# Performance work log

Measured on AMD Instinct MI355X. Metric: run time of the kernel, lower is better.

The kernel has to match this reference:

```python
import jax, jax.numpy as jnp
import numpy as np
import math

B, R, D = 1, 2, 256
NH, NL, NP, ZA = 8, 1, 8, 4
H = W = 128
Q = H * W
HD = D // NH


def _bilinear(v, loc, Hl, Wl):
    # v: [BH, Hl*Wl, hd]; loc: [BH, Q, P, 2] normalized to [0,1]
    x = loc[..., 0] * Wl - 0.5
    y = loc[..., 1] * Hl - 0.5
    x0f = jnp.floor(x); y0f = jnp.floor(y)
    wx = (x - x0f)[..., None]; wy = (y - y0f)[..., None]
    x0 = x0f.astype(jnp.int32); y0 = y0f.astype(jnp.int32)
    def corner(iy, ix):
        valid = (iy >= 0) & (iy < Hl) & (ix >= 0) & (ix < Wl)
        idx = jnp.clip(iy, 0, Hl - 1) * Wl + jnp.clip(ix, 0, Wl - 1)
        g = jax.vmap(lambda vb, ib: vb[ib])(v, idx)  # [BH,Q,P,hd]
        return g * valid[..., None].astype(v.dtype)
    g00 = corner(y0, x0); g01 = corner(y0, x0 + 1)
    g10 = corner(y0 + 1, x0); g11 = corner(y0 + 1, x0 + 1)
    return (g00 * (1 - wx) + g01 * wx) * (1 - wy) + (g10 * (1 - wx) + g11 * wx) * wy


def setup_inputs() -> dict:
    key = jax.random.key(0)
    ks = jax.random.split(key, 12)
    query = jax.random.normal(ks[0], (B, Q, D), jnp.float32)
    value = jax.random.normal(ks[1], (B * R, Q, D), jnp.float32)
    reference_points = jax.random.uniform(ks[2], (R, Q, ZA, 2), jnp.float32)
    spatial_shapes = jnp.array([[H, W]], jnp.int32)
    # sampling_offsets: zero-ish weight + directional grid bias (as in init_weights)
    W_off = 0.01 * jax.random.normal(ks[3], (NH * NL * NP * 2, D), jnp.float32)
    thetas = jnp.arange(NH, dtype=jnp.float32) * (2.0 * math.pi / NH)
    grid = jnp.stack([jnp.cos(thetas), jnp.sin(thetas)], -1)
    grid = grid / jnp.max(jnp.abs(grid), axis=-1, keepdims=True)
    grid = jnp.tile(grid[:, None, None, :], (1, NL, NP, 1))
    grid = grid * (jnp.arange(1, NP + 1, dtype=jnp.float32)[None, None, :, None])
    b_off = grid.reshape(-1)
    W_attn = 0.01 * jax.random.normal(ks[4], (NH * NL * NP, D), jnp.float32)
    b_attn = 0.01 * jax.random.normal(ks[5], (NH * NL * NP,), jnp.float32)
    s = 1.0 / np.sqrt(D)
    W_val = s * jax.random.normal(ks[6], (D, D), jnp.float32)
    b_val = jnp.zeros((D,), jnp.float32)
    W_out = s * jax.random.normal(ks[7], (D, D), jnp.float32)
    b_out = jnp.zeros((D,), jnp.float32)
    return {"query": query, "value": value, "reference_points": reference_points,
            "spatial_shapes": spatial_shapes, "W_off": W_off, "b_off": b_off,
            "W_attn": W_attn, "b_attn": b_attn, "W_val": W_val, "b_val": b_val,
            "W_out": W_out, "b_out": b_out}


def reference(query, value, reference_points, spatial_shapes,
              W_off, b_off, W_attn, b_attn, W_val, b_val, W_out, b_out):
    shapes = np.asarray(spatial_shapes)  # static level shapes
    residual = query
    Bq, nq, d = query.shape
    Rr, _, za, _ = reference_points.shape
    # rebatch query/reference_points over histories -> batch Bq*Rr (== value batch)
    q = jnp.broadcast_to(query[:, None], (Bq, Rr, nq, d)).reshape(Bq * Rr, nq, d)
    rp = jnp.broadcast_to(reference_points[None], (Bq, Rr, nq, za, 2)).reshape(Bq * Rr, nq, za, 2)
    bs = value.shape[0]
    v = (value @ W_val.T + b_val).reshape(bs, -1, NH, HD)
    off = (q @ W_off.T + b_off).reshape(bs, nq, NH, NL, NP, 2)
    aw = jax.nn.softmax((q @ W_attn.T + b_attn).reshape(bs, nq, NH, NL * NP), axis=-1)
    aw = aw.reshape(bs, nq, NH, NL, NP)
    norm = jnp.stack([shapes[:, 1].astype(np.float32), shapes[:, 0].astype(np.float32)], -1)  # [NL,2] = (W,H)
    off = off / norm[None, None, None, :, None, :]
    off = off.reshape(bs, nq, NH, NL, NP // za, za, 2)
    loc = rp[:, :, None, None, None, :, :] + off  # [bs,nq,NH,NL,NP//za,za,2]
    loc = loc.reshape(bs, nq, NH, NL, NP, 2)
    # multi-scale deformable attention (gather + bilinear + weighted sum)
    starts = np.concatenate([[0], np.cumsum(shapes[:, 0] * shapes[:, 1])])
    out = jnp.zeros((bs * NH, nq, HD), v.dtype)
    for l in range(NL):
        Hl, Wl = int(shapes[l, 0]), int(shapes[l, 1])
        vl = v[:, starts[l]:starts[l + 1]].transpose(0, 2, 1, 3).reshape(bs * NH, Hl * Wl, HD)
        locl = loc[:, :, :, l].transpose(0, 2, 1, 3, 4).reshape(bs * NH, nq, NP, 2)
        sampled = _bilinear(vl, locl, Hl, Wl)  # [bs*NH, nq, NP, hd]
        awl = aw[:, :, :, l].transpose(0, 2, 1, 3).reshape(bs * NH, nq, NP)
        out = out + jnp.einsum('bqph,bqp->bqh', sampled, awl)
    out = out.reshape(bs, NH, nq, HD).transpose(0, 2, 1, 3).reshape(bs, nq, d)
    out = out.mean(0, keepdims=True)  # mean over history-batch dim -> [1,nq,d]
    out = out @ W_out.T + b_out
    return out + residual  # dropout is identity in eval
```

## Files before the change

### kernel.cpp

```cpp
#include <hip/hip_runtime.h>
#include <hip/hip_bf16.h>
#include <hip/hip_fp16.h>
#include <hip/hip_fp8.h>

#define QN 16384
#define DK 256

typedef float f4_t __attribute__((ext_vector_type(4)));
typedef float f2_t __attribute__((ext_vector_type(2)));
typedef short s16x8 __attribute__((ext_vector_type(8)));
typedef short s16x4 __attribute__((ext_vector_type(4)));
typedef unsigned int u32;
typedef u32 u32x4 __attribute__((ext_vector_type(4)));
typedef u32 u32x2 __attribute__((ext_vector_type(2)));
typedef __fp16 h2_t __attribute__((ext_vector_type(2)));

__device__ inline short f2bf(float f){
  __hip_bfloat16 h = __float2bfloat16(f);
  return __builtin_bit_cast(short, h);
}
__device__ inline u32 pk2h(float a, float b){
#if __has_builtin(__builtin_amdgcn_cvt_pkrtz)
  h2_t r = __builtin_amdgcn_cvt_pkrtz(a, b);
  return __builtin_bit_cast(u32, r);
#else
  return (u32)__builtin_bit_cast(unsigned short, __float2half(a)) |
         ((u32)__builtin_bit_cast(unsigned short, __float2half(b)) << 16);
#endif
}
__device__ inline u32 pk_fp8(float a, float b){
#if __has_builtin(__builtin_amdgcn_cvt_pk_fp8_f32)
  return (u32)__builtin_amdgcn_cvt_pk_fp8_f32(a, b, 0, false);
#else
  __hip_fp8_e4m3 fa(a), fb(b);
  return (u32)fa.__x | ((u32)fb.__x << 8);
#endif
}
template<bool HI>
__device__ inline f2_t upk_fp8(u32 w){
#if __has_builtin(__builtin_amdgcn_cvt_pk_f32_fp8)
  return __builtin_amdgcn_cvt_pk_f32_fp8(w, HI);
#else
  const u32 hh = HI ? (w >> 16) : (w & 0xFFFFu);
  __hip_fp8_e4m3 a, b;
  a.__x = (unsigned char)(hh & 0xFF);
  b.__x = (unsigned char)(hh >> 8);
  return (f2_t){(float)a, (float)b};
#endif
}
__device__ inline s16x8 ldw8(const float* __restrict__ src){
  const f4_t v0 = *(const f4_t*)src;
  const f4_t v1 = *(const f4_t*)(src + 4);
  s16x8 o = { f2bf(v0[0]), f2bf(v0[1]), f2bf(v0[2]), f2bf(v0[3]),
              f2bf(v1[0]), f2bf(v1[1]), f2bf(v1[2]), f2bf(v1[3]) };
  return o;
}

__global__ __launch_bounds__(256, 2) void k_proj(const float* __restrict__ value,
    const float* __restrict__ query, const float* __restrict__ Wval,
    const float* __restrict__ Woff, const float* __restrict__ Wattn,
    const float* __restrict__ bval, const float* __restrict__ boff,
    const float* __restrict__ battn, char* __restrict__ vfp8,
    float* __restrict__ offw, float* __restrict__ logit){
  __shared__ short As[64 * 256];
  __shared__ short Bs[64 * 256];
  __shared__ u32 Cs[64 * 16];
  const int tid = threadIdx.x;
  const int lane = tid & 63, wv = tid >> 6;
  const int r16 = lane & 15, kh = lane >> 4;
  const int swsel = (r16 & 7) << 4;
  const int bid = blockIdx.x;

  if (bid < 512){
    const float* A = value;
    const int mbase = bid * 64;
    #pragma unroll
    for (int i = 0; i < 16; ++i){
      const int lin = i * 256 + tid;
      const int r = lin >> 6, ck = lin & 63;
      const f4_t v = *(const f4_t*)(A + (size_t)(mbase + r) * DK + ck * 4);
      s16x4 o = { f2bf(v[0]), f2bf(v[1]), f2bf(v[2]), f2bf(v[3]) };
      *(s16x4*)((char*)As + r * 512 + ((ck * 8) ^ ((r & 7) << 4))) = o;
    }
    s16x8 breg[8];
    #pragma unroll
    for (int i = 0; i < 8; ++i){
      const int lin = i * 256 + tid;
      const int n = lin >> 5, ck = lin & 31;
      breg[i] = ldw8(Wval + (size_t)n * DK + ck * 8);
    }
    __syncthreads();
    for (int cg = 0; cg < 4; ++cg){
      #pragma unroll
      for (int i = 0; i < 8; ++i){
        const int lin = i * 256 + tid;
        const int n = lin >> 5, ck = lin & 31;
        *(s16x8*)((char*)Bs + n * 512 + ((ck * 16) ^ ((n & 7) << 4))) = breg[i];
      }
      __syncthreads();
      if (cg < 3){
        #pragma unroll
        for (int i = 0; i < 8; ++i){
          const int lin = i * 256 + tid;
          const int n = lin >> 5, ck = lin & 31;
          breg[i] = ldw8(Wval + (size_t)((cg + 1) * 64 + n) * DK + ck * 8);
        }
      }
      f4_t acc[4];
      #pragma unroll
      for (int i = 0; i < 4; ++i) acc[i] = (f4_t){0.f, 0.f, 0.f, 0.f};
      #pragma unroll
      for (int kk = 0; kk < 8; ++kk){
        const int kb = kh * 16 + kk * 64;
        const s16x8 a = *(const s16x8*)((char*)As + (wv * 16 + r16) * 512 + (kb ^ swsel));
        #pragma unroll
        for (int nt = 0; nt < 4; ++nt){
          const s16x8 b = *(const s16x8*)((char*)Bs + (nt * 16 + r16) * 512 + (kb ^ swsel));
          acc[nt] = __builtin_amdgcn_mfma_f32_16x16x32_bf16(a, b, acc[nt], 0, 0, 0);
        }
      }
      #pragma unroll
      for (int nt = 0; nt < 4; ++nt){
        const int n = cg * 64 + nt * 16 + r16;
        const float bv = bval[n];
        #pragma unroll
        for (int rix = 0; rix < 4; ++rix){
          const float vv = acc[nt][rix] + bv;
          ((char*)Cs)[(wv * 16 + kh * 4 + rix) * 64 + nt * 16 + r16] =
              (char)(pk_fp8(vv, 0.f) & 0xFFu);
        }
      }
      __syncthreads();
      {
        const u32x4 cw = *((const u32x4*)((const char*)Cs + tid * 16));
        const int pixl = tid >> 2, q4 = tid & 3;
        const int h2 = cg * 2 + (q4 >> 1);
        const int m = mbase + pixl;
        const int r = m >> 14, pix = m & (QN - 1);
        *(u32x4*)(vfp8 + ((size_t)((r * 8 + h2) * QN + pix)) * 32 + (q4 & 1) * 16) = cw;
      }
    }
  } else {
    const float* A = query;
    const int mg = wv & 1, ch = wv >> 1;
    const int mbase = (bid - 512) * 32;
    #pragma unroll
    for (int i = 0; i < 8; ++i){
      const int lin = i * 256 + tid;
      const int r = lin >> 6, ck = lin & 63;
      const f4_t v = *(const f4_t*)(A + (size_t)(mbase + r) * DK + ck * 4);
      s16x4 o = { f2bf(v[0]), f2bf(v[1]), f2bf(v[2]), f2bf(v[3]) };
      *(s16x4*)((char*)As + r * 512 + ((ck * 8) ^ ((r & 7) << 4))) = o;
    }
    s16x8 breg[8];
    #pragma unroll
    for (int i = 0; i < 8; ++i){
      const int lin = i * 256 + tid;
      const int n = lin >> 5, ck = lin & 31;
      breg[i] = ldw8(Woff + (size_t)n * DK + ck * 8);
    }
    __syncthreads();
    for (int cg = 0; cg < 3; ++cg){
      #pragma unroll
      for (int i = 0; i < 8; ++i){
        const int lin = i * 256 + tid;
        const int n = lin >> 5, ck = lin & 31;
        *(s16x8*)((char*)Bs + n * 512 + ((ck * 16) ^ ((n & 7) << 4))) = breg[i];
      }
      __syncthreads();
      if (cg < 2){
        #pragma unroll
        for (int i = 0; i < 8; ++i){
          const int lin = i * 256 + tid;
          const int n = lin >> 5, ck = lin & 31;
          const int rrow = (cg + 1) * 64 + n;
          const float* src = (rrow < 128) ? (Woff  + (size_t)rrow * DK)
                                          : (Wattn + (size_t)(rrow - 128) * DK);
          breg[i] = ldw8(src + ck * 8);
        }
      }
      f4_t acc[2];
      acc[0] = (f4_t){0.f,0.f,0.f,0.f}; acc[1] = (f4_t){0.f,0.f,0.f,0.f};
      #pragma unroll
      for (int kk = 0; kk < 8; ++kk){
        const int kb = kh * 16 + kk * 64;
        const s16x8 a = *(const s16x8*)((char*)As + (mg * 16 + r16) * 512 + (kb ^ swsel));
        #pragma unroll
        for (int nt = 0; nt < 2; ++nt){
          const s16x8 b = *(const s16x8*)((char*)Bs + (ch * 32 + nt * 16 + r16) * 512 + (kb ^ swsel));
          acc[nt] = __builtin_amdgcn_mfma_f32_16x16x32_bf16(a, b, acc[nt], 0, 0, 0);
        }
      }
      #pragma unroll
      for (int nt = 0; nt < 2; ++nt){
        const int n = cg * 64 + ch * 32 + nt * 16 + r16;
        #pragma unroll
        for (int rix = 0; rix < 4; ++rix){
          const int m = mbase + mg * 16 + kh * 4 + rix;
          const float v = acc[nt][rix];
          if (n < 128) offw[(size_t)m * 128 + n] = v + boff[n];
          else         logit[(size_t)m * 64 + (n - 128)] = v + battn[n - 128];
        }
      }
      __syncthreads();
    }
  }
}

__global__ __launch_bounds__(256, 2) void k_gemm_out(const short* __restrict__ Ab,
    const float* __restrict__ Wout, const float* __restrict__ bout,
    const float* __restrict__ query, float* __restrict__ out){
  __shared__ short As[32 * 256];
  __shared__ short Bs[64 * 256];
  const int tid = threadIdx.x;
  const int lane = tid & 63, wv = tid >> 6;
  const int r16 = lane & 15, kh = lane >> 4;
  const int mg = wv & 1, ch = wv >> 1;
  const int swsel = (r16 & 7) << 4;
  const int mbase = blockIdx.x * 32;

  #pragma unroll
  for (int i = 0; i < 4; ++i){
    const int lin = i * 256 + tid;
    const int r = lin >> 5, ck = lin & 31;
    const s16x8 v = *(const s16x8*)(Ab + (size_t)(mbase + r) * DK + ck * 8);
    *(s16x8*)((char*)As + r * 512 + ((ck * 16) ^ ((r & 7) << 4))) = v;
  }
  s16x8 breg[8];
  #pragma unroll
  for (int i = 0; i < 8; ++i){
    const int lin = i * 256 + tid;
    const int n = lin >> 5, ck = lin & 31;
    breg[i] = ldw8(Wout + (size_t)n * DK + ck * 8);
  }
  __syncthreads();

  for (int cg = 0; cg < 4; ++cg){
    #pragma unroll
    for (int i = 0; i < 8; ++i){
      const int lin = i * 256 + tid;
      const int n = lin >> 5, ck = lin & 31;
      *(s16x8*)((char*)Bs + n * 512 + ((ck * 16) ^ ((n & 7) << 4))) = breg[i];
    }
    __syncthreads();
    if (cg < 3){
      #pragma unroll
      for (int i = 0; i < 8; ++i){
        const int lin = i * 256 + tid;
        const int n = lin >> 5, ck = lin & 31;
        breg[i] = ldw8(Wout + (size_t)((cg + 1) * 64 + n) * DK + ck * 8);
      }
    }
    f4_t acc[2];
    acc[0] = (f4_t){0.f,0.f,0.f,0.f}; acc[1] = (f4_t){0.f,0.f,0.f,0.f};
    #pragma unroll
    for (int kk = 0; kk < 8; ++kk){
      const int kb = kh * 16 + kk * 64;
      const s16x8 a = *(const s16x8*)((char*)As + (mg * 16 + r16) * 512 + (kb ^ swsel));
      #pragma unroll
      for (int nt = 0; nt < 2; ++nt){
        const s16x8 b = *(const s16x8*)((char*)Bs + (ch * 32 + nt * 16 + r16) * 512 + (kb ^ swsel));
        acc[nt] = __builtin_amdgcn_mfma_f32_16x16x32_bf16(a, b, acc[nt], 0, 0, 0);
      }
    }
    #pragma unroll
    for (int nt = 0; nt < 2; ++nt){
      const int n = cg * 64 + ch * 32 + nt * 16 + r16;
      const float bo = bout[n];
      #pragma unroll
      for (int rix = 0; rix < 4; ++rix){
        const int m = mbase + mg * 16 + kh * 4 + rix;
        out[(size_t)m * DK + n] = acc[nt][rix] + bo + query[(size_t)m * DK + n];
      }
    }
    __syncthreads();
  }
}

__device__ inline void mkw(float rx, float ry, float ox, float oy, float awp,
                           u32& word, u32& pk01, u32& pk23){
  const float x = fmaf(rx, 128.f, ox) - 0.5f;
  const float y = fmaf(ry, 128.f, oy) - 0.5f;
  const float xf = floorf(x), yf = floorf(y);
  const float wx = x - xf, wy = y - yf;
  const int ix = (int)xf, iy = (int)yf;
  float xw0 = 1.f - wx, xw1 = wx, yw0 = 1.f - wy, yw1 = wy;
  if (ix < 0 || ix > 127)   xw0 = 0.f;
  if (ix < -1 || ix > 126)  xw1 = 0.f;
  if (iy < 0 || iy > 127)   yw0 = 0.f;
  if (iy < -1 || iy > 126)  yw1 = 0.f;
  const int ix0 = min(max(ix, 0), 127), ix1 = min(max(ix + 1, 0), 127);
  const int iy0 = min(max(iy, 0), 127), iy1 = min(max(iy + 1, 0), 127);
  const float t0 = awp * yw0, t1 = awp * yw1;
  pk01 = pk2h(t0 * xw0, t0 * xw1);
  pk23 = pk2h(t1 * xw0, t1 * xw1);
  word = (u32)(iy0 * 128 + ix0) | ((u32)(ix1 - ix0) << 16) | ((u32)(iy1 - iy0) << 17);
}

__global__ __launch_bounds__(256) void k_sampler(const float* __restrict__ rp,
    const float* __restrict__ offw, const float* __restrict__ logit,
    const char* __restrict__ vfp8, short* __restrict__ O2b){
  const int tid = threadIdx.x;
  const int j3 = tid & 7;
  const int row2 = j3 >> 2;
  const int px2 = (j3 >> 1) & 1;
  const int ck2 = j3 & 1;
  const int grp = tid >> 3;
  const int lane = tid & 63;
  const int glane8 = lane & ~7;
  const int h = blockIdx.x & 7;
  const int q = (blockIdx.x >> 3) * 32 + grp;
  const u32 laneof = (u32)ck2 * 16;

  const float* lp = logit + (size_t)q * 64 + h * 8;
  const float l = lp[j3];
  float m = l;
  m = fmaxf(m, __shfl_xor(m, 1)); m = fmaxf(m, __shfl_xor(m, 2)); m = fmaxf(m, __shfl_xor(m, 4));
  const float e = __expf(l - m);
  float ssum = e;
  ssum += __shfl_xor(ssum, 1); ssum += __shfl_xor(ssum, 2); ssum += __shfl_xor(ssum, 4);
  const float awp = e * (0.5f / ssum);

  const float* offp = offw + (size_t)q * 128 + h * 16;
  const float ox = offp[2 * j3], oy = offp[2 * j3 + 1];
  const int za2 = (j3 & 3) * 2;
  const float rx0 = rp[(size_t)q * 8 + za2],        ry0 = rp[(size_t)q * 8 + za2 + 1];
  const float rx1 = rp[(size_t)(QN + q) * 8 + za2], ry1 = rp[(size_t)(QN + q) * 8 + za2 + 1];

  u32 wrdA, pkA01, pkA23, wrdB, pkB01, pkB23;
  mkw(rx0, ry0, ox, oy, awp, wrdA, pkA01, pkA23);
  mkw(rx1, ry1, ox, oy, awp, wrdB, pkB01, pkB23);

  const char* vb0 = vfp8 + (size_t)(h * QN) * 32;
  const char* vb1 = vfp8 + (size_t)((8 + h) * QN) * 32;

  float acc[16];
  #pragma unroll
  for (int i = 0; i < 16; ++i) acc[i] = 0.f;

#define LOADP(S, WRD, VB)                                                   \
  const u32 wd_##S = __shfl((WRD), glane8 | ((S) & 7));                     \
  const u32 ad_##S = (wd_##S & 0xFFFFu) * 32u + laneof                      \
                   + (px2 ? ((wd_##S >> 11) & 32u) : 0u)                    \
                   + (row2 ? ((wd_##S >> 17) & 1u) * 4096u : 0u);           \
  const u32x4 c_##S = *(const u32x4*)((VB) + ad_##S);

#define USEP(S, PK01, PK23) do{                                             \
    const int srcl_ = glane8 | ((S) & 7);                                   \
    const u32 w01_ = __shfl((PK01), srcl_);                                 \
    const u32 w23_ = __shfl((PK23), srcl_);                                 \
    const u32 wsel_ = row2 ? w23_ : w01_;                                   \
    const h2_t wh_ = __builtin_bit_cast(h2_t, wsel_);                       \
    const float w_ = px2 ? (float)wh_[1] : (float)wh_[0];                   \
    _Pragma("unroll")                                                       \
    for (int i_ = 0; i_ < 4; ++i_){                                         \
      const f2_t lo_ = upk_fp8<false>(c_##S[i_]);                           \
      const f2_t hi_ = upk_fp8<true >(c_##S[i_]);                           \
      acc[4*i_+0] = fmaf(w_, lo_[0], acc[4*i_+0]);                          \
      acc[4*i_+1] = fmaf(w_, lo_[1], acc[4*i_+1]);                          \
      acc[4*i_+2] = fmaf(w_, hi_[0], acc[4*i_+2]);                          \
      acc[4*i_+3] = fmaf(w_, hi_[1], acc[4*i_+3]);                          \
    }                                                                       \
  }while(0)

  LOADP(0,  wrdA, vb0) LOADP(1,  wrdA, vb0) LOADP(2,  wrdA, vb0)
  USEP(0,  pkA01, pkA23); LOADP(3,  wrdA, vb0)
  USEP(1,  pkA01, pkA23); LOADP(4,  wrdA, vb0)
  USEP(2,  pkA01, pkA23); LOADP(5,  wrdA, vb0)
  USEP(3,  pkA01, pkA23); LOADP(6,  wrdA, vb0)
  USEP(4,  pkA01, pkA23); LOADP(7,  wrdA, vb0)
  USEP(5,  pkA01, pkA23); LOADP(8,  wrdB, vb1)
  USEP(6,  pkA01, pkA23); LOADP(9,  wrdB, vb1)
  USEP(7,  pkA01, pkA23); LOADP(10, wrdB, vb1)
  USEP(8,  pkB01, pkB23); LOADP(11, wrdB, vb1)
  USEP(9,  pkB01, pkB23); LOADP(12, wrdB, vb1)
  USEP(10, pkB01, pkB23); LOADP(13, wrdB, vb1)
  USEP(11, pkB01, pkB23); LOADP(14, wrdB, vb1)
  USEP(12, pkB01, pkB23); LOADP(15, wrdB, vb1)
  USEP(13, pkB01, pkB23);
  USEP(14, pkB01, pkB23);
  USEP(15, pkB01, pkB23);
#undef LOADP
#undef USEP

  #pragma unroll
  for (int i = 0; i < 16; ++i) acc[i] += __shfl_xor(acc[i], 4);
  #pragma unroll
  for (int i = 0; i < 16; ++i) acc[i] += __shfl_xor(acc[i], 2);
  if (j3 < 2){
    short* op = O2b + (size_t)q * DK + h * 32 + j3 * 16;
    s16x8 o0 = { f2bf(acc[0]),  f2bf(acc[1]),  f2bf(acc[2]),  f2bf(acc[3]),
                 f2bf(acc[4]),  f2bf(acc[5]),  f2bf(acc[6]),  f2bf(acc[7]) };
    s16x8 o1 = { f2bf(acc[8]),  f2bf(acc[9]),  f2bf(acc[10]), f2bf(acc[11]),
                 f2bf(acc[12]), f2bf(acc[13]), f2bf(acc[14]), f2bf(acc[15]) };
    *(s16x8*)op       = o0;
    *(s16x8*)(op + 8) = o1;
  }
}

extern "C" void kernel_launch(void* const* d_in, const int* in_sizes, int n_in,
                              void* d_out, int out_size, void* d_ws, size_t ws_size,
                              hipStream_t stream) {
  const float* query = (const float*)d_in[0];
  const float* value = (const float*)d_in[1];
  const float* refpt = (const float*)d_in[2];
  const float* W_off  = (const float*)d_in[4];
  const float* b_off  = (const float*)d_in[5];
  const float* W_attn = (const float*)d_in[6];
  const float* b_attn = (const float*)d_in[7];
  const float* W_val  = (const float*)d_in[8];
  const float* b_val  = (const float*)d_in[9];
  const float* W_out  = (const float*)d_in[10];
  const float* b_out  = (const float*)d_in[11];
  float* out = (float*)d_out;

  char* ws = (char*)d_ws;
  char*  vfp8 = (char*)(ws);
  float* offw = (float*)(ws + 8388608);
  float* logit= (float*)(ws + 16777216);
  short* O2b  = (short*)(ws + 20971520);

  k_proj    <<<dim3(1024), dim3(256), 0, stream>>>(value, query, W_val, W_off, W_attn,
                                                   b_val, b_off, b_attn, vfp8, offw, logit);
  k_sampler <<<dim3(4096), dim3(256), 0, stream>>>(refpt, offw, logit, vfp8, O2b);
  k_gemm_out<<<dim3(512),  dim3(256), 0, stream>>>(O2b, W_out, b_out, query, out);
}
```

Measured before the change: 67.60 us.

## Prepack weights into MFMA fragment layout and read B operands from global

After: 75.15 us. +11.2%, slower.

```diff
diff --git a/kernel.cpp b/kernel.cpp
--- a/kernel.cpp
+++ b/kernel.cpp
@@ -56,14 +56,29 @@
   return o;
 }
 
-__global__ __launch_bounds__(256, 2) void k_proj(const float* __restrict__ value,
-    const float* __restrict__ query, const float* __restrict__ Wval,
-    const float* __restrict__ Woff, const float* __restrict__ Wattn,
+__global__ __launch_bounds__(256) void k_wprep(const float* __restrict__ Wv,
+    const float* __restrict__ Wo, const float* __restrict__ Wa,
+    const float* __restrict__ Wt, short* __restrict__ Wp){
+  const int idx = blockIdx.x * 256 + threadIdx.x;
+  const int t = idx >> 9;
+  const int kk = (idx >> 6) & 7;
+  const int lane = idx & 63;
+  const int r16 = lane & 15, kh = lane >> 4;
+  const int row = t * 16 + r16;
+  const float* src;
+  if (row < 256)      src = Wv + (size_t)row * DK;
+  else if (row < 384) src = Wo + (size_t)(row - 256) * DK;
+  else if (row < 448) src = Wa + (size_t)(row - 384) * DK;
+  else                src = Wt + (size_t)(row - 448) * DK;
+  *(s16x8*)(Wp + (size_t)idx * 8) = ldw8(src + kh * 8 + kk * 32);
+}
+
+__global__ __launch_bounds__(256, 4) void k_proj(const float* __restrict__ value,
+    const float* __restrict__ query, const short* __restrict__ Wp,
     const float* __restrict__ bval, const float* __restrict__ boff,
     const float* __restrict__ battn, char* __restrict__ vfp8,
     float* __restrict__ offw, float* __restrict__ logit){
   __shared__ short As[64 * 256];
-  __shared__ short Bs[64 * 256];
   __shared__ u32 Cs[64 * 16];
   const int tid = threadIdx.x;
   const int lane = tid & 63, wv = tid >> 6;
@@ -72,51 +87,33 @@
   const int bid = blockIdx.x;
 
   if (bid < 512){
-    const float* A = value;
     const int mbase = bid * 64;
     #pragma unroll
     for (int i = 0; i < 16; ++i){
       const int lin = i * 256 + tid;
       const int r = lin >> 6, ck = lin & 63;
-      const f4_t v = *(const f4_t*)(A + (size_t)(mbase + r) * DK + ck * 4);
+      const f4_t v = *(const f4_t*)(value + (size_t)(mbase + r) * DK + ck * 4);
       s16x4 o = { f2bf(v[0]), f2bf(v[1]), f2bf(v[2]), f2bf(v[3]) };
       *(s16x4*)((char*)As + r * 512 + ((ck * 8) ^ ((r & 7) << 4))) = o;
     }
-    s16x8 breg[8];
-    #pragma unroll
-    for (int i = 0; i < 8; ++i){
-      const int lin = i * 256 + tid;
-      const int n = lin >> 5, ck = lin & 31;
-      breg[i] = ldw8(Wval + (size_t)n * DK + ck * 8);
-    }
     __syncthreads();
+    s16x8 af[8];
+    #pragma unroll
+    for (int kk = 0; kk < 8; ++kk){
+      const int kb = kh * 16 + kk * 64;
+      af[kk] = *(const s16x8*)((char*)As + (wv * 16 + r16) * 512 + (kb ^ swsel));
+    }
     for (int cg = 0; cg < 4; ++cg){
-      #pragma unroll
-      for (int i = 0; i < 8; ++i){
-        const int lin = i * 256 + tid;
-        const int n = lin >> 5, ck = lin & 31;
-        *(s16x8*)((char*)Bs + n * 512 + ((ck * 16) ^ ((n & 7) << 4))) = breg[i];
-      }
-      __syncthreads();
-      if (cg < 3){
-        #pragma unroll
-        for (int i = 0; i < 8; ++i){
-          const int lin = i * 256 + tid;
-          const int n = lin >> 5, ck = lin & 31;
-          breg[i] = ldw8(Wval + (size_t)((cg + 1) * 64 + n) * DK + ck * 8);
-        }
-      }
       f4_t acc[4];
       #pragma unroll
       for (int i = 0; i < 4; ++i) acc[i] = (f4_t){0.f, 0.f, 0.f, 0.f};
       #pragma unroll
       for (int kk = 0; kk < 8; ++kk){
-        const int kb = kh * 16 + kk * 64;
-        const s16x8 a = *(const s16x8*)((char*)As + (wv * 16 + r16) * 512 + (kb ^ swsel));
         #pragma unroll
         for (int nt = 0; nt < 4; ++nt){
-          const s16x8 b = *(const s16x8*)((char*)Bs + (nt * 16 + r16) * 512 + (kb ^ swsel));
-          acc[nt] = __builtin_amdgcn_mfma_f32_16x16x32_bf16(a, b, acc[nt], 0, 0, 0);
+          const s16x8 b = *(const s16x8*)(Wp +
+              (size_t)((((cg * 4 + nt) * 8 + kk) * 64) + lane) * 8);
+          acc[nt] = __builtin_amdgcn_mfma_f32_16x16x32_bf16(af[kk], b, acc[nt], 0, 0, 0);
         }
       }
       #pragma unroll
@@ -139,56 +136,38 @@
         const int r = m >> 14, pix = m & (QN - 1);
         *(u32x4*)(vfp8 + ((size_t)((r * 8 + h2) * QN + pix)) * 32 + (q4 & 1) * 16) = cw;
       }
+      __syncthreads();
     }
   } else {
-    const float* A = query;
     const int mg = wv & 1, ch = wv >> 1;
     const int mbase = (bid - 512) * 32;
+    const short* Wpo = Wp + (size_t)16 * 8 * 64 * 8;
     #pragma unroll
     for (int i = 0; i < 8; ++i){
       const int lin = i * 256 + tid;
       const int r = lin >> 6, ck = lin & 63;
-      const f4_t v = *(const f4_t*)(A + (size_t)(mbase + r) * DK + ck * 4);
+      const f4_t v = *(const f4_t*)(query + (size_t)(mbase + r) * DK + ck * 4);
       s16x4 o = { f2bf(v[0]), f2bf(v[1]), f2bf(v[2]), f2bf(v[3]) };
       *(s16x4*)((char*)As + r * 512 + ((ck * 8) ^ ((r & 7) << 4))) = o;
     }
-    s16x8 breg[8];
-    #pragma unroll
-    for (int i = 0; i < 8; ++i){
-      const int lin = i * 256 + tid;
-      const int n = lin >> 5, ck = lin & 31;
-      breg[i] = ldw8(Woff + (size_t)n * DK + ck * 8);
-    }
     __syncthreads();
+    s16x8 af[8];
+    #pragma unroll
+    for (int kk = 0; kk < 8; ++kk){
+      const int kb = kh * 16 + kk * 64;
+      af[kk] = *(const s16x8*)((char*)As + (mg * 16 + r16) * 512 + (kb ^ swsel));
+    }
     for (int cg = 0; cg < 3; ++cg){
-      #pragma unroll
-      for (int i = 0; i < 8; ++i){
-        const int lin = i * 256 + tid;
-        const int n = lin >> 5, ck = lin & 31;
-        *(s16x8*)((char*)Bs + n * 512 + ((ck * 16) ^ ((n & 7) << 4))) = breg[i];
-      }
-      __syncthreads();
-      if (cg < 2){
-        #pragma unroll
-        for (int i = 0; i < 8; ++i){
-          const int lin = i * 256 + tid;
-          const int n = lin >> 5, ck = lin & 31;
-          const int rrow = (cg + 1) * 64 + n;
-          const float* src = (rrow < 128) ? (Woff  + (size_t)rrow * DK)
-                                          : (Wattn + (size_t)(rrow - 128) * DK);
-          breg[i] = ldw8(src + ck * 8);
-        }
-      }
       f4_t acc[2];
       acc[0] = (f4_t){0.f,0.f,0.f,0.f}; acc[1] = (f4_t){0.f,0.f,0.f,0.f};
       #pragma unroll
       for (int kk = 0; kk < 8; ++kk){
-        const int kb = kh * 16 + kk * 64;
-        const s16x8 a = *(const s16x8*)((char*)As + (mg * 16 + r16) * 512 + (kb ^ swsel));
         #pragma unroll
         for (int nt = 0; nt < 2; ++nt){
-          const s16x8 b = *(const s16x8*)((char*)Bs + (ch * 32 + nt * 16 + r16) * 512 + (kb ^ swsel));
-          acc[nt] = __builtin_amdgcn_mfma_f32_16x16x32_bf16(a, b, acc[nt], 0, 0, 0);
+          const int tl = cg * 4 + ch * 2 + nt;
+          const s16x8 b = *(const s16x8*)(Wpo +
+              (size_t)(((tl * 8 + kk) * 64) + lane) * 8);
+          acc[nt] = __builtin_amdgcn_mfma_f32_16x16x32_bf16(af[kk], b, acc[nt], 0, 0, 0);
         }
       }
       #pragma unroll
@@ -202,22 +181,21 @@
           else         logit[(size_t)m * 64 + (n - 128)] = v + battn[n - 128];
         }
       }
-      __syncthreads();
     }
   }
 }
 
 __global__ __launch_bounds__(256, 2) void k_gemm_out(const short* __restrict__ Ab,
-    const float* __restrict__ Wout, const float* __restrict__ bout,
+    const short* __restrict__ Wp, const float* __restrict__ bout,
     const float* __restrict__ query, float* __restrict__ out){
   __shared__ short As[32 * 256];
-  __shared__ short Bs[64 * 256];
   const int tid = threadIdx.x;
   const int lane = tid & 63, wv = tid >> 6;
   const int r16 = lane & 15, kh = lane >> 4;
   const int mg = wv & 1, ch = wv >> 1;
   const int swsel = (r16 & 7) << 4;
   const int mbase = blockIdx.x * 32;
+  const short* Wpt = Wp + (size_t)28 * 8 * 64 * 8;
 
   #pragma unroll
   for (int i = 0; i < 4; ++i){
@@ -226,41 +204,24 @@
     const s16x8 v = *(const s16x8*)(Ab + (size_t)(mbase + r) * DK + ck * 8);
     *(s16x8*)((char*)As + r * 512 + ((ck * 16) ^ ((r & 7) << 4))) = v;
   }
-  s16x8 breg[8];
-  #pragma unroll
-  for (int i = 0; i < 8; ++i){
-    const int lin = i * 256 + tid;
-    const int n = lin >> 5, ck = lin & 31;
-    breg[i] = ldw8(Wout + (size_t)n * DK + ck * 8);
-  }
   __syncthreads();
-
+  s16x8 af[8];
+  #pragma unroll
+  for (int kk = 0; kk < 8; ++kk){
+    const int kb = kh * 16 + kk * 64;
+    af[kk] = *(const s16x8*)((char*)As + (mg * 16 + r16) * 512 + (kb ^ swsel));
+  }
   for (int cg = 0; cg < 4; ++cg){
-    #pragma unroll
-    for (int i = 0; i < 8; ++i){
-      const int lin = i * 256 + tid;
-      const int n = lin >> 5, ck = lin & 31;
-      *(s16x8*)((char*)Bs + n * 512 + ((ck * 16) ^ ((n & 7) << 4))) = breg[i];
-    }
-    __syncthreads();
-    if (cg < 3){
-      #pragma unroll
-      for (int i = 0; i < 8; ++i){
-        const int lin = i * 256 + tid;
-        const int n = lin >> 5, ck = lin & 31;
-        breg[i] = ldw8(Wout + (size_t)((cg + 1) * 64 + n) * DK + ck * 8);
-      }
-    }
     f4_t acc[2];
     acc[0] = (f4_t){0.f,0.f,0.f,0.f}; acc[1] = (f4_t){0.f,0.f,0.f,0.f};
     #pragma unroll
     for (int kk = 0; kk < 8; ++kk){
-      const int kb = kh * 16 + kk * 64;
-      const s16x8 a = *(const s16x8*)((char*)As + (mg * 16 + r16) * 512 + (kb ^ swsel));
       #pragma unroll
       for (int nt = 0; nt < 2; ++nt){
-        const s16x8 b = *(const s16x8*)((char*)Bs + (ch * 32 + nt * 16 + r16) * 512 + (kb ^ swsel));
-        acc[nt] = __builtin_amdgcn_mfma_f32_16x16x32_bf16(a, b, acc[nt], 0, 0, 0);
+        const int tl = cg * 4 + ch * 2 + nt;
+        const s16x8 b = *(const s16x8*)(Wpt +
+            (size_t)(((tl * 8 + kk) * 64) + lane) * 8);
+        acc[nt] = __builtin_amdgcn_mfma_f32_16x16x32_bf16(af[kk], b, acc[nt], 0, 0, 0);
       }
     }
     #pragma unroll
@@ -273,7 +234,6 @@
         out[(size_t)m * DK + n] = acc[nt][rix] + bo + query[(size_t)m * DK + n];
       }
     }
-    __syncthreads();
   }
 }
 
@@ -415,13 +375,15 @@
   float* out = (float*)d_out;
 
   char* ws = (char*)d_ws;
-  char*  vfp8 = (char*)(ws);
-  float* offw = (float*)(ws + 8388608);
-  float* logit= (float*)(ws + 16777216);
-  short* O2b  = (short*)(ws + 20971520);
-
-  k_proj    <<<dim3(1024), dim3(256), 0, stream>>>(value, query, W_val, W_off, W_attn,
-                                                   b_val, b_off, b_attn, vfp8, offw, logit);
+  short* Wp   = (short*)(ws);
+  char*  vfp8 = (char*)(ws + 360448);
+  float* offw = (float*)(ws + 8749056);
+  float* logit= (float*)(ws + 17137664);
+  short* O2b  = (short*)(ws + 21331968);
+
+  k_wprep   <<<dim3(88),   dim3(256), 0, stream>>>(W_val, W_off, W_attn, W_out, Wp);
+  k_proj    <<<dim3(1024), dim3(256), 0, stream>>>(value, query, Wp, b_val, b_off,
+                                                   b_attn, vfp8, offw, logit);
   k_sampler <<<dim3(4096), dim3(256), 0, stream>>>(refpt, offw, logit, vfp8, O2b);
-  k_gemm_out<<<dim3(512),  dim3(256), 0, stream>>>(O2b, W_out, b_out, query, out);
-}
+  k_gemm_out<<<dim3(512),  dim3(256), 0, stream>>>(O2b, Wp, b_out, query, out);
+}
```
